# Performance work log

Hardware: AMD Instinct MI355X
Metric: run time of the kernel (lower is better)

The kernel has to match this reference:

```python
import jax, jax.numpy as jnp
import numpy as np

N_NODES = 100000
N_EDGES = 1600000
D = 128
N_LAYERS = 3  # GIN num_layers = n_layers + 1 with n_layers = 2
BN_EPS = 1e-5


def _batchnorm(x, gamma, beta):
    # Training-mode BatchNorm1d over the node axis (biased variance, as torch uses
    # for normalization).
    mean = jnp.mean(x, axis=0)
    var = jnp.mean((x - mean) ** 2, axis=0)
    return (x - mean) * jax.lax.rsqrt(var + BN_EPS) * gamma + beta


def setup_inputs() -> dict:
    key = jax.random.key(0)
    ks = jax.random.split(key, 5)
    features = jax.random.normal(ks[0], (N_NODES, D), dtype=jnp.float32)
    W = jax.random.normal(ks[1], (N_LAYERS, D, D), dtype=jnp.float32) * 0.05
    b = jnp.zeros((N_LAYERS, D), dtype=jnp.float32)
    eps = jnp.zeros((N_LAYERS,), dtype=jnp.float32)  # learn_eps init 0
    bn1_gamma = jnp.ones((N_LAYERS, D), dtype=jnp.float32)
    bn1_beta = jnp.zeros((N_LAYERS, D), dtype=jnp.float32)
    bn2_gamma = jnp.ones((N_LAYERS, D), dtype=jnp.float32)
    bn2_beta = jnp.zeros((N_LAYERS, D), dtype=jnp.float32)
    src = jax.random.randint(ks[2], (N_EDGES,), 0, N_NODES, dtype=jnp.int64 if jax.config.jax_enable_x64 else jnp.int32)
    dst = jax.random.randint(ks[3], (N_EDGES,), 0, N_NODES, dtype=jnp.int64 if jax.config.jax_enable_x64 else jnp.int32)
    return {
        'features': features, 'W': W, 'b': b, 'eps': eps,
        'bn1_gamma': bn1_gamma, 'bn1_beta': bn1_beta,
        'bn2_gamma': bn2_gamma, 'bn2_beta': bn2_beta,
        'src': src, 'dst': dst,
    }


def reference(features, W, b, eps, bn1_gamma, bn1_beta, bn2_gamma, bn2_beta, src, dst):
    n = features.shape[0]
    h = features
    hidden_rep = [h]
    for i in range(N_LAYERS):
        # GINConv, 'sum' aggregation: (1+eps)*h_v + sum_{u->v} h_u
        agg = jax.ops.segment_sum(h[src], dst, num_segments=n)
        z = (1.0 + eps[i]) * h + agg
        # ApplyNodeFunc: Linear (num_mlp_layers=1) -> BN -> ReLU
        z = z @ W[i] + b[i]
        z = jax.nn.relu(_batchnorm(z, bn1_gamma[i], bn1_beta[i]))
        # GIN.forward: outer BN -> ReLU
        z = jax.nn.relu(_batchnorm(z, bn2_gamma[i], bn2_beta[i]))
        h = z
        hidden_rep.append(h)
    # torch.stack(hidden_rep) -> [n_layers+2, N, D]
    return jnp.stack(hidden_rep, axis=0)
```

## Files before the change

kernel.cpp:

```cpp
#include <hip/hip_runtime.h>
#include <hip/hip_bf16.h>

#define DD 128

typedef __attribute__((ext_vector_type(8))) short bfrag8;
typedef __attribute__((ext_vector_type(4))) float f32x4;

__device__ __forceinline__ float bf16lo(unsigned int u) {
    union { unsigned int i; float f; } c; c.i = u << 16; return c.f;
}
__device__ __forceinline__ float bf16hi(unsigned int u) {
    union { unsigned int i; float f; } c; c.i = u & 0xffff0000u; return c.f;
}
__device__ __forceinline__ float bf16f(unsigned short u) {
    union { unsigned int i; float f; } c; c.i = ((unsigned int)u) << 16; return c.f;
}
__device__ __forceinline__ unsigned short f2bf(float f) {
    union { float f; unsigned int i; } c; c.f = f;
    unsigned int x = c.i;
    unsigned int r = (x + 0x7fffu + ((x >> 16) & 1u)) >> 16;
    return (unsigned short)r;
}

__global__ void k_setup(const int* __restrict__ dst, int* __restrict__ deg, int E,
                        const float* __restrict__ features, float* __restrict__ out0,
                        unsigned int* __restrict__ hb, int total4,
                        const float* __restrict__ W, unsigned short* __restrict__ Wt) {
    int gtid = blockIdx.x * blockDim.x + threadIdx.x;
    int gsz = gridDim.x * blockDim.x;
    for (int i = gtid; i < E; i += gsz) atomicAdd(&deg[dst[i]], 1);
    for (int i = gtid; i < total4; i += gsz) {
        float4 v = ((const float4*)features)[i];
        ((float4*)out0)[i] = v;
        unsigned int lo = (unsigned int)f2bf(v.x) | ((unsigned int)f2bf(v.y) << 16);
        unsigned int hi = (unsigned int)f2bf(v.z) | ((unsigned int)f2bf(v.w) << 16);
        ((uint2*)hb)[i] = make_uint2(lo, hi);
    }
    for (int i = gtid; i < 3 * 128 * 128; i += gsz) {
        int l = i >> 14, r = i & 16383, k = r >> 7, n = r & 127;
        Wt[(l << 14) + n * 128 + k] = f2bf(W[i]);
    }
}

__global__ void k_scan1(const int* __restrict__ deg, int* __restrict__ partials, int Nn) {
    __shared__ int sm[256];
    int tid = threadIdx.x;
    int base = (blockIdx.x << 10) + 4 * tid;
    int s = 0;
    if (base + 3 < Nn) {
        int4 v = *(const int4*)&deg[base];
        s = v.x + v.y + v.z + v.w;
    } else {
        for (int j = 0; j < 4; j++) if (base + j < Nn) s += deg[base + j];
    }
    sm[tid] = s;
    __syncthreads();
    for (int off = 128; off > 0; off >>= 1) {
        if (tid < off) sm[tid] += sm[tid + off];
        __syncthreads();
    }
    if (tid == 0) partials[blockIdx.x] = sm[0];
}

__global__ void k_scan3(const int* __restrict__ deg, const int* __restrict__ partials,
                        int* __restrict__ row_start, int Nn, int E, int nchunk) {
    __shared__ int sp[256];
    __shared__ int sm[256];
    int tid = threadIdx.x, c = blockIdx.x;
    int p = (tid < nchunk) ? partials[tid] : 0;
    sp[tid] = p;
    __syncthreads();
    for (int off = 1; off < 256; off <<= 1) {
        int t = (tid >= off) ? sp[tid - off] : 0;
        __syncthreads();
        sp[tid] += t;
        __syncthreads();
    }
    int chunkpref = (c == 0) ? 0 : sp[c - 1];

    int base = (c << 10) + 4 * tid;
    int d0 = 0, d1 = 0, d2 = 0, d3 = 0;
    if (base + 3 < Nn) {
        int4 v = *(const int4*)&deg[base];
        d0 = v.x; d1 = v.y; d2 = v.z; d3 = v.w;
    } else {
        if (base + 0 < Nn) d0 = deg[base + 0];
        if (base + 1 < Nn) d1 = deg[base + 1];
        if (base + 2 < Nn) d2 = deg[base + 2];
        if (base + 3 < Nn) d3 = deg[base + 3];
    }
    int ts = d0 + d1 + d2 + d3;
    sm[tid] = ts;
    __syncthreads();
    for (int off = 1; off < 256; off <<= 1) {
        int t = (tid >= off) ? sm[tid - off] : 0;
        __syncthreads();
        sm[tid] += t;
        __syncthreads();
    }
    int run = chunkpref + sm[tid] - ts;
    if (base + 0 < Nn) row_start[base + 0] = run; run += d0;
    if (base + 1 < Nn) row_start[base + 1] = run; run += d1;
    if (base + 2 < Nn) row_start[base + 2] = run; run += d2;
    if (base + 3 < Nn) row_start[base + 3] = run;
    if (c == 0 && tid == 0) row_start[Nn] = E;
}

__global__ void k_scatter(const int* __restrict__ src, const int* __restrict__ dst,
                          const int* __restrict__ row_start, int* __restrict__ cursor,
                          int* __restrict__ csr, int E) {
    int i = blockIdx.x * blockDim.x + threadIdx.x;
    if (i < E) {
        int d = dst[i];
        int pos = row_start[d] + atomicAdd(&cursor[d], 1);
        csr[pos] = src[i];
    }
}

__global__ void k_gather(const unsigned int* __restrict__ hb, const int* __restrict__ row_start,
                         const int* __restrict__ csr, const float* __restrict__ eps, int layer,
                         unsigned int* __restrict__ zb, int Nn) {
    int wv = threadIdx.x >> 6, lane = threadIdx.x & 63;
    int v = blockIdx.x * 4 + wv;
    if (v >= Nn) return;
    float e1 = 1.0f + eps[layer];
    unsigned int hs = hb[(size_t)v * 64 + lane];
    float ax = e1 * bf16lo(hs);
    float ay = e1 * bf16hi(hs);
    int beg = row_start[v], end = row_start[v + 1];
    int e = beg;
    for (; e + 7 < end; e += 8) {
        int u0 = csr[e], u1 = csr[e + 1], u2 = csr[e + 2], u3 = csr[e + 3];
        int u4 = csr[e + 4], u5 = csr[e + 5], u6 = csr[e + 6], u7 = csr[e + 7];
        unsigned int h0 = hb[(size_t)u0 * 64 + lane];
        unsigned int h1 = hb[(size_t)u1 * 64 + lane];
        unsigned int h2 = hb[(size_t)u2 * 64 + lane];
        unsigned int h3 = hb[(size_t)u3 * 64 + lane];
        unsigned int h4 = hb[(size_t)u4 * 64 + lane];
        unsigned int h5 = hb[(size_t)u5 * 64 + lane];
        unsigned int h6 = hb[(size_t)u6 * 64 + lane];
        unsigned int h7 = hb[(size_t)u7 * 64 + lane];
        ax += bf16lo(h0) + bf16lo(h1) + bf16lo(h2) + bf16lo(h3)
            + bf16lo(h4) + bf16lo(h5) + bf16lo(h6) + bf16lo(h7);
        ay += bf16hi(h0) + bf16hi(h1) + bf16hi(h2) + bf16hi(h3)
            + bf16hi(h4) + bf16hi(h5) + bf16hi(h6) + bf16hi(h7);
    }
    for (; e < end; e++) {
        unsigned int hu = hb[(size_t)csr[e] * 64 + lane];
        ax += bf16lo(hu); ay += bf16hi(hu);
    }
    zb[(size_t)v * 64 + lane] = (unsigned int)f2bf(ax) | ((unsigned int)f2bf(ay) << 16);
}

__launch_bounds__(256)
__global__ void k_gemm(const unsigned short* __restrict__ zb, const unsigned short* __restrict__ Wt,
                       const float* __restrict__ bias, int layer, unsigned short* __restrict__ yb,
                       float* __restrict__ stl, int Nn) {
    __shared__ unsigned short Al[64 * 136];
    int tid = threadIdx.x;
    int m0 = blockIdx.x * 64;
    #pragma unroll
    for (int p = 0; p < 4; p++) {
        int slot = p * 256 + tid;
        int r = slot >> 4, c = slot & 15;
        int grow = m0 + r;
        uint4 val = make_uint4(0, 0, 0, 0);
        if (grow < Nn) val = *(const uint4*)&zb[(size_t)grow * 128 + c * 8];
        *(uint4*)&Al[r * 136 + c * 8] = val;
    }
    __syncthreads();

    int lane = tid & 63, wv = tid >> 6;
    int tcol = lane & 15, quad = lane >> 4;
    const unsigned short* Wl = Wt + (layer << 14);
    f32x4 acc[4][2];
    #pragma unroll
    for (int a = 0; a < 4; a++)
        #pragma unroll
        for (int b2 = 0; b2 < 2; b2++) acc[a][b2] = (f32x4){0.f, 0.f, 0.f, 0.f};

    #pragma unroll
    for (int kk = 0; kk < 128; kk += 32) {
        int kb = kk + quad * 8;
        bfrag8 af[4], bf[2];
        #pragma unroll
        for (int mt = 0; mt < 4; mt++)
            af[mt] = *(const bfrag8*)&Al[(16 * mt + tcol) * 136 + kb];
        #pragma unroll
        for (int nt = 0; nt < 2; nt++)
            bf[nt] = *(const bfrag8*)&Wl[(32 * wv + 16 * nt + tcol) * 128 + kb];
        #pragma unroll
        for (int mt = 0; mt < 4; mt++)
            #pragma unroll
            for (int nt = 0; nt < 2; nt++)
                acc[mt][nt] = __builtin_amdgcn_mfma_f32_16x16x32_bf16(af[mt], bf[nt], acc[mt][nt], 0, 0, 0);
    }

    #pragma unroll
    for (int nt = 0; nt < 2; nt++) {
        int col = 32 * wv + 16 * nt + tcol;
        float bcol = bias[layer * 128 + col];
        float psum = 0.f, psq = 0.f;
        #pragma unroll
        for (int mt = 0; mt < 4; mt++) {
            #pragma unroll
            for (int r = 0; r < 4; r++) {
                int row = m0 + 16 * mt + quad * 4 + r;
                if (row < Nn) {
                    unsigned short u = f2bf(acc[mt][nt][r] + bcol);
                    yb[(size_t)row * 128 + col] = u;
                    float vr = bf16f(u);
                    psum += vr;
                    psq += vr * vr;
                }
            }
        }
        psum += __shfl_xor(psum, 16); psq += __shfl_xor(psq, 16);
        psum += __shfl_xor(psum, 32); psq += __shfl_xor(psq, 32);
        if (lane < 16) {
            atomicAdd(&stl[col], psum);
            atomicAdd(&stl[128 + col], psq);
        }
    }
}

__launch_bounds__(256)
__global__ void k_stats2(const unsigned short* __restrict__ yb, float* __restrict__ stl,
                         const float* __restrict__ g1, const float* __restrict__ b1,
                         int layer, int totalU8, float invN) {
    __shared__ float red[512];
    int tid = threadIdx.x;
    if (tid < 128) {
        float m = stl[tid] * invN;
        float var = stl[128 + tid] * invN - m * m;
        float rstd = rsqrtf(var + 1e-5f);
        float s = g1[layer * 128 + tid] * rstd;
        red[tid] = s;
        red[128 + tid] = b1[layer * 128 + tid] - m * s;
        red[256 + tid] = 0.f;
        red[384 + tid] = 0.f;
    }
    __syncthreads();
    int lane = tid & 63;
    int cbase = (8 * tid) & 127;
    float s1r[8], sh1r[8];
    #pragma unroll
    for (int j = 0; j < 8; j++) { s1r[j] = red[cbase + j]; sh1r[j] = red[128 + cbase + j]; }
    float ps[8], pq[8];
    #pragma unroll
    for (int j = 0; j < 8; j++) { ps[j] = 0.f; pq[j] = 0.f; }
    int gtid = blockIdx.x * 256 + tid;
    int gsz = gridDim.x * 256;
    const uint4* yb4 = (const uint4*)yb;
    for (int i = gtid; i < totalU8; i += gsz) {
        uint4 v = yb4[i];
        float f[8];
        f[0] = bf16lo(v.x); f[1] = bf16hi(v.x);
        f[2] = bf16lo(v.y); f[3] = bf16hi(v.y);
        f[4] = bf16lo(v.z); f[5] = bf16hi(v.z);
        f[6] = bf16lo(v.w); f[7] = bf16hi(v.w);
        #pragma unroll
        for (int j = 0; j < 8; j++) {
            float t = fmaxf(f[j] * s1r[j] + sh1r[j], 0.f);
            ps[j] += t; pq[j] += t * t;
        }
    }
    #pragma unroll
    for (int j = 0; j < 8; j++) {
        ps[j] += __shfl_xor(ps[j], 16);
        pq[j] += __shfl_xor(pq[j], 16);
        ps[j] += __shfl_xor(ps[j], 32);
        pq[j] += __shfl_xor(pq[j], 32);
    }
    if (lane < 16) {
        #pragma unroll
        for (int j = 0; j < 8; j++) {
            atomicAdd(&red[256 + cbase + j], ps[j]);
            atomicAdd(&red[384 + cbase + j], pq[j]);
        }
    }
    __syncthreads();
    if (tid < 128) {
        atomicAdd(&stl[256 + tid], red[256 + tid]);
        atomicAdd(&stl[384 + tid], red[384 + tid]);
    }
}

__launch_bounds__(256)
__global__ void k_apply(const unsigned short* __restrict__ yb, const float* __restrict__ stl,
                        const float* __restrict__ g1, const float* __restrict__ b1,
                        const float* __restrict__ g2, const float* __restrict__ b2,
                        int layer, float* __restrict__ outl, unsigned int* __restrict__ hb,
                        int totalU8, float invN) {
    __shared__ float red[512];
    int tid = threadIdx.x;
    if (tid < 128) {
        float m1 = stl[tid] * invN;
        float v1 = stl[128 + tid] * invN - m1 * m1;
        float r1 = rsqrtf(v1 + 1e-5f);
        float s1 = g1[layer * 128 + tid] * r1;
        red[tid] = s1;
        red[128 + tid] = b1[layer * 128 + tid] - m1 * s1;
        float m2 = stl[256 + tid] * invN;
        float v2 = stl[384 + tid] * invN - m2 * m2;
        float r2 = rsqrtf(v2 + 1e-5f);
        float s2 = g2[layer * 128 + tid] * r2;
        red[256 + tid] = s2;
        red[384 + tid] = b2[layer * 128 + tid] - m2 * s2;
    }
    __syncthreads();
    int cbase = (8 * tid) & 127;
    float s1a[8], sh1a[8], s2a[8], sh2a[8];
    #pragma unroll
    for (int j = 0; j < 8; j++) {
        s1a[j]  = red[cbase + j];       sh1a[j] = red[128 + cbase + j];
        s2a[j]  = red[256 + cbase + j]; sh2a[j] = red[384 + cbase + j];
    }
    int gtid = blockIdx.x * 256 + tid;
    int gsz = gridDim.x * 256;
    const uint4* yb4 = (const uint4*)yb;
    for (int i = gtid; i < totalU8; i += gsz) {
        uint4 v = yb4[i];
        float f[8];
        f[0] = bf16lo(v.x); f[1] = bf16hi(v.x);
        f[2] = bf16lo(v.y); f[3] = bf16hi(v.y);
        f[4] = bf16lo(v.z); f[5] = bf16hi(v.z);
        f[6] = bf16lo(v.w); f[7] = bf16hi(v.w);
        float o[8];
        #pragma unroll
        for (int j = 0; j < 8; j++) {
            float t = fmaxf(f[j] * s1a[j] + sh1a[j], 0.f);
            o[j] = fmaxf(t * s2a[j] + sh2a[j], 0.f);
        }
        ((float4*)outl)[2 * i]     = make_float4(o[0], o[1], o[2], o[3]);
        ((float4*)outl)[2 * i + 1] = make_float4(o[4], o[5], o[6], o[7]);
        uint4 hbv;
        hbv.x = (unsigned int)f2bf(o[0]) | ((unsigned int)f2bf(o[1]) << 16);
        hbv.y = (unsigned int)f2bf(o[2]) | ((unsigned int)f2bf(o[3]) << 16);
        hbv.z = (unsigned int)f2bf(o[4]) | ((unsigned int)f2bf(o[5]) << 16);
        hbv.w = (unsigned int)f2bf(o[6]) | ((unsigned int)f2bf(o[7]) << 16);
        ((uint4*)hb)[i] = hbv;
    }
}

extern "C" void kernel_launch(void* const* d_in, const int* in_sizes, int n_in,
                              void* d_out, int out_size, void* d_ws, size_t ws_size,
                              hipStream_t stream) {
    const float* features = (const float*)d_in[0];
    const float* W        = (const float*)d_in[1];
    const float* bias     = (const float*)d_in[2];
    const float* eps      = (const float*)d_in[3];
    const float* g1       = (const float*)d_in[4];
    const float* b1       = (const float*)d_in[5];
    const float* g2       = (const float*)d_in[6];
    const float* b2       = (const float*)d_in[7];
    const int*   src      = (const int*)d_in[8];
    const int*   dst      = (const int*)d_in[9];

    const int Nn = in_sizes[0] / DD;
    const int E  = in_sizes[8];
    float* out = (float*)d_out;

    char* w = (char*)d_ws;
    auto alloc = [&](size_t bytes) -> char* {
        char* p = w;
        w += (bytes + 255) & ~(size_t)255;
        return p;
    };
    int*   deg    = (int*)alloc((size_t)Nn * 4);
    int*   cursor = (int*)alloc((size_t)Nn * 4);
    float* stats  = (float*)alloc(3 * 512 * 4);
    char*  zero_end = w;
    int* row_start = (int*)alloc((size_t)(Nn + 1) * 4);
    int* partials  = (int*)alloc(1024);
    int* csr       = (int*)alloc((size_t)E * 4);
    unsigned int* hb = (unsigned int*)alloc((size_t)Nn * 64 * 4);
    unsigned int* zb = (unsigned int*)alloc((size_t)Nn * 64 * 4);
    unsigned short* Wt = (unsigned short*)alloc((size_t)3 * 128 * 128 * 2);
    unsigned short* yb = (unsigned short*)alloc((size_t)Nn * 128 * 2);

    const int total4 = Nn * DD / 4;
    const int totalU8 = Nn * DD / 8;
    const float invN = 1.0f / (float)Nn;
    const int nchunk = (Nn + 1023) / 1024;

    hipMemsetAsync(deg, 0, (size_t)(zero_end - (char*)deg), stream);

    k_setup<<<(E + 255) / 256, 256, 0, stream>>>(dst, deg, E, features, out, hb, total4, W, Wt);
    k_scan1<<<nchunk, 256, 0, stream>>>(deg, partials, Nn);
    k_scan3<<<nchunk, 256, 0, stream>>>(deg, partials, row_start, Nn, E, nchunk);
    k_scatter<<<(E + 255) / 256, 256, 0, stream>>>(src, dst, row_start, cursor, csr, E);

    for (int l = 0; l < 3; l++) {
        float* stl = stats + l * 512;
        float* outl = out + (size_t)(l + 1) * Nn * DD;
        k_gather<<<(Nn + 3) / 4, 256, 0, stream>>>(hb, row_start, csr, eps, l, zb, Nn);
        k_gemm<<<(Nn + 63) / 64, 256, 0, stream>>>((const unsigned short*)zb, Wt, bias, l, yb,
                                                   stl, Nn);
        k_stats2<<<512, 256, 0, stream>>>(yb, stl, g1, b1, l, totalU8, invN);
        k_apply<<<1024, 256, 0, stream>>>(yb, stl, g1, b1, g2, b2, l, outl, hb, totalU8, invN);
    }
}
```

Baseline: 863.8 us.

## Split gather by feature column slices so each block covers 64 nodes

The gather kernel is reorganized so each block handles one 32-byte column slice (of 8) across 64 nodes, with 4 lanes per node each loading a uint2. The intent is to shrink the per-pass working set of the feature table so that slices stay resident in cache, and to let each wave serve 16 nodes rather than one, which improves latency hiding. The trade-off is that each CSR row is now read 8 times and the feature rows are fetched as small 32-byte segments, with a shallower unroll of 4.

```diff
diff --git a/kernel.cpp b/kernel.cpp
--- a/kernel.cpp
+++ b/kernel.cpp
@@ -120,36 +120,43 @@
 __global__ void k_gather(const unsigned int* __restrict__ hb, const int* __restrict__ row_start,
                          const int* __restrict__ csr, const float* __restrict__ eps, int layer,
                          unsigned int* __restrict__ zb, int Nn) {
-    int wv = threadIdx.x >> 6, lane = threadIdx.x & 63;
-    int v = blockIdx.x * 4 + wv;
+    int bid = blockIdx.x;
+    int cs = bid & 7;
+    int nb = bid >> 3;
+    int tid = threadIdx.x;
+    int wv = tid >> 6, lane = tid & 63;
+    int grp = lane >> 2;
+    int sub = lane & 3;
+    int v = nb * 64 + wv * 16 + grp;
     if (v >= Nn) return;
     float e1 = 1.0f + eps[layer];
-    unsigned int hs = hb[(size_t)v * 64 + lane];
-    float ax = e1 * bf16lo(hs);
-    float ay = e1 * bf16hi(hs);
-    int beg = row_start[v], end = row_start[v + 1];
-    int e = beg;
-    for (; e + 7 < end; e += 8) {
+    const uint2* hb2 = (const uint2*)hb;
+    int sb = cs * 4 + sub;
+    uint2 hs = hb2[(size_t)v * 32 + sb];
+    float a0 = e1 * bf16lo(hs.x), a1 = e1 * bf16hi(hs.x);
+    float a2 = e1 * bf16lo(hs.y), a3 = e1 * bf16hi(hs.y);
+    int e = row_start[v], end = row_start[v + 1];
+    for (; e + 3 < end; e += 4) {
         int u0 = csr[e], u1 = csr[e + 1], u2 = csr[e + 2], u3 = csr[e + 3];
-        int u4 = csr[e + 4], u5 = csr[e + 5], u6 = csr[e + 6], u7 = csr[e + 7];
-        unsigned int h0 = hb[(size_t)u0 * 64 + lane];
-        unsigned int h1 = hb[(size_t)u1 * 64 + lane];
-        unsigned int h2 = hb[(size_t)u2 * 64 + lane];
-        unsigned int h3 = hb[(size_t)u3 * 64 + lane];
-        unsigned int h4 = hb[(size_t)u4 * 64 + lane];
-        unsigned int h5 = hb[(size_t)u5 * 64 + lane];
-        unsigned int h6 = hb[(size_t)u6 * 64 + lane];
-        unsigned int h7 = hb[(size_t)u7 * 64 + lane];
-        ax += bf16lo(h0) + bf16lo(h1) + bf16lo(h2) + bf16lo(h3)
-            + bf16lo(h4) + bf16lo(h5) + bf16lo(h6) + bf16lo(h7);
-        ay += bf16hi(h0) + bf16hi(h1) + bf16hi(h2) + bf16hi(h3)
-            + bf16hi(h4) + bf16hi(h5) + bf16hi(h6) + bf16hi(h7);
+        uint2 x0 = hb2[(size_t)u0 * 32 + sb];
+        uint2 x1 = hb2[(size_t)u1 * 32 + sb];
+        uint2 x2 = hb2[(size_t)u2 * 32 + sb];
+        uint2 x3 = hb2[(size_t)u3 * 32 + sb];
+        a0 += bf16lo(x0.x) + bf16lo(x1.x) + bf16lo(x2.x) + bf16lo(x3.x);
+        a1 += bf16hi(x0.x) + bf16hi(x1.x) + bf16hi(x2.x) + bf16hi(x3.x);
+        a2 += bf16lo(x0.y) + bf16lo(x1.y) + bf16lo(x2.y) + bf16lo(x3.y);
+        a3 += bf16hi(x0.y) + bf16hi(x1.y) + bf16hi(x2.y) + bf16hi(x3.y);
     }
     for (; e < end; e++) {
-        unsigned int hu = hb[(size_t)csr[e] * 64 + lane];
-        ax += bf16lo(hu); ay += bf16hi(hu);
-    }
-    zb[(size_t)v * 64 + lane] = (unsigned int)f2bf(ax) | ((unsigned int)f2bf(ay) << 16);
+        int u = csr[e];
+        uint2 x = hb2[(size_t)u * 32 + sb];
+        a0 += bf16lo(x.x); a1 += bf16hi(x.x);
+        a2 += bf16lo(x.y); a3 += bf16hi(x.y);
+    }
+    uint2 o;
+    o.x = (unsigned int)f2bf(a0) | ((unsigned int)f2bf(a1) << 16);
+    o.y = (unsigned int)f2bf(a2) | ((unsigned int)f2bf(a3) << 16);
+    ((uint2*)zb)[(size_t)v * 32 + sb] = o;
 }
 
 __launch_bounds__(256)
@@ -394,7 +401,7 @@
     for (int l = 0; l < 3; l++) {
         float* stl = stats + l * 512;
         float* outl = out + (size_t)(l + 1) * Nn * DD;
-        k_gather<<<(Nn + 3) / 4, 256, 0, stream>>>(hb, row_start, csr, eps, l, zb, Nn);
+        k_gather<<<((Nn + 63) / 64) * 8, 256, 0, stream>>>(hb, row_start, csr, eps, l, zb, Nn);
         k_gemm<<<(Nn + 63) / 64, 256, 0, stream>>>((const unsigned short*)zb, Wt, bias, l, yb,
                                                    stl, Nn);
         k_stats2<<<512, 256, 0, stream>>>(yb, stl, g1, b1, l, totalU8, invN);
```

Result: slower. 1.259 ms (+45.8%).
